# Kernel optimization log

Hardware: AMD Instinct MI355X
Metric: run time of the kernel (lower is better)

The kernel has to match this reference:

```python
import jax, jax.numpy as jnp
import numpy as np

K = 15  # window_size


def setup_inputs() -> dict:
    key = jax.random.key(0)
    k1, k2, k3, k4 = jax.random.split(key, 4)
    x = jax.random.normal(k1, (8, 256, 240, 240), dtype=jnp.float32)
    wq = jax.random.normal(k2, (144, 256), dtype=jnp.float32) * (1.0 / np.sqrt(256))
    wk = jax.random.normal(k3, (144, 256), dtype=jnp.float32) * (1.0 / np.sqrt(256))
    wproj = jax.random.normal(k4, (256, 256), dtype=jnp.float32) * (1.0 / np.sqrt(256))
    return {"x": x, "wq": wq, "wk": wk, "wproj": wproj}


def _pnlm(x, wq, wk, wproj):
    b, c, h, w = x.shape
    ph, pw = (-h) % K, (-w) % K
    if ph or pw:
        x_pad = jnp.pad(x, ((0, 0), (0, 0), (0, ph), (0, pw)), mode='reflect')
    else:
        x_pad = x
    H, W = x_pad.shape[2], x_pad.shape[3]
    nh, nw = H // K, W // K
    N = K * K  # tokens per window
    # blockify: (B,C,H,W) -> (B*nh*nw, C, N)
    blocks = (x_pad.reshape(b, c, nh, K, nw, K)
              .transpose(0, 2, 4, 1, 3, 5)
              .reshape(b * nh * nw, c, N))
    q = jnp.einsum('ec,bcn->bne', wq, blocks)   # (B', N, E)
    km = jnp.einsum('ec,bcm->bem', wk, blocks)  # (B', E, N)
    att = jnp.einsum('bne,bem->bnm', q, km)     # (B', N, N)
    scale = 1.0 / jnp.sqrt(jnp.asarray(q.shape[-1], dtype=att.dtype))
    att = jax.nn.softmax(att * scale, axis=-1)
    y = jnp.einsum('bnm,bcm->bcn', att, blocks)  # att @ V, V = blocks^T
    y = jnp.einsum('oc,bcn->bon', wproj, y)      # 1x1 proj_out
    # unblockify: (B', C, N) -> (B, C, H, W)
    y = (y.reshape(b, nh, nw, c, K, K)
         .transpose(0, 3, 1, 4, 2, 5)
         .reshape(b, c, H, W))
    y = y[:, :, :h, :w]
    return x + y


def reference(x, wq, wk, wproj):
    return _pnlm(x, wq, wk, wproj)
```

## Files before the change

### kernel.cpp

```cpp
#include <hip/hip_runtime.h>


typedef __bf16 bf16x8 __attribute__((ext_vector_type(8)));
typedef float  f32x4  __attribute__((ext_vector_type(4)));

#define MFMA(a,b,c) __builtin_amdgcn_mfma_f32_16x16x32_bf16((a),(b),(c),0,0,0)

#define QK_ROW 320
#define KL_STRIDE 168
#define XBB_ROW 240

__device__ __forceinline__ unsigned short f2bf(float f){
  union { float f; unsigned int u; } v; v.f = f;
  unsigned int r = v.u + 0x7FFFu + ((v.u >> 16) & 1u);
  return (unsigned short)(r >> 16);
}
__device__ __forceinline__ float bf2f(unsigned short u){
  union { unsigned int u; float f; } v; v.u = ((unsigned int)u) << 16;
  return v.f;
}
__device__ __forceinline__ int swz(int row, int col){
  return row*256 + ((((col >> 3) ^ (row & 7)) << 3) | (col & 7));
}
__device__ __forceinline__ int swzC(int row, int col){
  return row*256 + (col ^ ((((row >> 3) ^ row) & 7) << 3));
}
__device__ __forceinline__ bf16x8 ld_frag_lds(const unsigned short* p, int idx){
  uint4 v = *(const uint4*)(p + idx);
  return __builtin_bit_cast(bf16x8, v);
}
__device__ __forceinline__ bf16x8 ld_frag_b(const void* p){
  uint4 v = *(const uint4*)(p);
  return __builtin_bit_cast(bf16x8, v);
}

__device__ __forceinline__ void repack_frag(const unsigned int* plo, const unsigned int* phi,
                                            uint4* outf, int lane){
  const int nn = lane & 15, hh = lane >> 4;
  const int sla = nn + 32*(hh & 1);
  const int slb = sla + 16;
  const bool up = hh >= 2;
  #pragma unroll
  for (int k = 0; k < 8; ++k){
    unsigned int a0 = (unsigned int)__shfl((int)plo[2*k],   sla);
    unsigned int a1 = (unsigned int)__shfl((int)plo[2*k+1], sla);
    unsigned int b0 = (unsigned int)__shfl((int)phi[2*k],   sla);
    unsigned int b1 = (unsigned int)__shfl((int)phi[2*k+1], sla);
    unsigned int c0 = (unsigned int)__shfl((int)plo[2*k],   slb);
    unsigned int c1 = (unsigned int)__shfl((int)plo[2*k+1], slb);
    unsigned int d0 = (unsigned int)__shfl((int)phi[2*k],   slb);
    unsigned int d1 = (unsigned int)__shfl((int)phi[2*k+1], slb);
    outf[k] = make_uint4(up?a1:a0, up?b1:b0, up?c1:c0, up?d1:d0);
  }
}

__global__ __launch_bounds__(256) void k_w(
    const float* __restrict__ wq, const float* __restrict__ wk,
    const float* __restrict__ wproj,
    unsigned short* __restrict__ wqb, unsigned short* __restrict__ wkb,
    unsigned short* __restrict__ wpb)
{
  int i = blockIdx.x*256 + threadIdx.x;
  if (i < 20480){
    int e = i >> 7, c = (i & 127)*2;
    unsigned int v = 0;
    if (e < 144) v = (unsigned int)f2bf(wq[e*256+c]) | ((unsigned int)f2bf(wq[e*256+c+1]) << 16);
    *(unsigned int*)(wqb + (size_t)i*2) = v;
  } else if (i < 40960){
    int j = i - 20480;
    int e = j >> 7, c = (j & 127)*2;
    unsigned int v = 0;
    if (e < 144) v = (unsigned int)f2bf(wk[e*256+c]) | ((unsigned int)f2bf(wk[e*256+c+1]) << 16);
    *(unsigned int*)(wkb + (size_t)j*2) = v;
  } else if (i < 73728){
    int l = i - 40960;
    int o = l >> 7, c = (l & 127)*2;
    *(unsigned int*)(wpb + (size_t)l*2) =
        (unsigned int)f2bf(wproj[o*256+c]) | ((unsigned int)f2bf(wproj[o*256+c+1]) << 16);
  }
}

__global__ __launch_bounds__(256) void k_xb(
    const float* __restrict__ x, unsigned short* __restrict__ xbb)
{
  __shared__ unsigned short xs[8*15*240];
  const int wg = blockIdx.x;
  const int cg = wg & 31;
  const int th = (wg >> 5) & 15;
  const int b  = wg >> 9;
  const int tid = threadIdx.x;

  const float* xb = x + ((size_t)b*256 + cg*8)*57600 + th*15*240;
  for (int i = tid; i < 8*15*120; i += 256){
    int c = i / 1800;
    int rem = i - c*1800;
    int r = rem / 120, p2 = rem - r*120;
    float2 v = *(const float2*)(xb + (size_t)c*57600 + r*240 + p2*2);
    *(unsigned int*)(&xs[(c*15 + r)*240 + p2*2]) =
        (unsigned int)f2bf(v.x) | ((unsigned int)f2bf(v.y) << 16);
  }
  __syncthreads();

  for (int i = tid; i < 8*16*30; i += 256){
    int c = i / 480;
    int rem = i - c*480;
    int tw = rem / 30, ch = rem - tw*30;
    union { unsigned short u16[8]; uint4 u4; } pk;
    #pragma unroll
    for (int j = 0; j < 8; ++j){
      int m = ch*8 + j;
      int r = m / 15, s = m - r*15;
      pk.u16[j] = (m <= 224) ? xs[(c*15 + r)*240 + tw*15 + s] : (unsigned short)0;
    }
    *(uint4*)(xbb + ((size_t)(b*256 + th*16 + tw)*256 + cg*8 + c)*XBB_ROW + ch*8) = pk.u4;
  }
}

__global__ __launch_bounds__(512,4) void k_fused(
    const unsigned short* __restrict__ xbb,
    const unsigned short* __restrict__ wqb, const unsigned short* __restrict__ wkb,
    const unsigned short* __restrict__ wpb,
    unsigned short* __restrict__ qkws, float* __restrict__ out)
{
  __shared__ __align__(16) unsigned short S[40960];
  unsigned short* xt  = S;
  unsigned short* wqs = S;
  unsigned short* wks = S + 8192;
  unsigned short* kl  = S;
  unsigned short* xl  = S;
  unsigned short* wl  = S;
  unsigned int*  hwp  = (unsigned int*)(S + 40320);
  const int wg = blockIdx.x;
  const int b  = wg >> 8;
  const int th = (wg >> 4) & 15, tw = wg & 15;
  const int h0 = th*15, w0 = tw*15;
  const int tid = threadIdx.x;
  const int lane = tid & 63, wave = tid >> 6;
  const int col  = lane & 15, hi = lane >> 4;
  const size_t obase = (size_t)b * 256 * 57600;
  const unsigned short* qkb = qkws + (size_t)b * 57600 * QK_ROW;
  const unsigned short* xbw = xbb + (size_t)wg * (256*XBB_ROW);

  if (tid < 240){
    int ms = tid <= 224 ? tid : 224;
    hwp[tid] = (unsigned int)((h0 + ms/15)*240 + w0 + ms%15);
  }

  bf16x8 af[2][8];
  #pragma unroll 1
  for (int half = 0; half < 2; ++half){
    if (half) __syncthreads();
    for (int i = tid; i < 256*16; i += 512){
      int c = i >> 4, m8 = i & 15;
      int m = half*128 + m8*8;
      if (m + 8 <= 240){
        uint4 v = *(const uint4*)(xbw + (size_t)c*XBB_ROW + m);
        const unsigned short* pv = (const unsigned short*)&v;
        #pragma unroll
        for (int j = 0; j < 8; ++j)
          xt[swzC(m8*8 + j, c)] = pv[j];
      }
    }
    __syncthreads();
    const int rloc = wave*16 + col;
    if (half == 0){
      #pragma unroll
      for (int k = 0; k < 8; ++k)
        af[0][k] = ld_frag_lds(xt, swzC(rloc, k*32 + hi*8));
    } else {
      #pragma unroll
      for (int k = 0; k < 8; ++k)
        af[1][k] = ld_frag_lds(xt, swzC(rloc, k*32 + hi*8));
    }
  }
  __syncthreads();

  #pragma unroll 1
  for (int eg = 0; eg < 5; ++eg){
    if (eg) __syncthreads();
    for (int i = tid; i < 32*32; i += 512){
      int e_l = i >> 5, c8 = (i & 31)*8;
      size_t off = (size_t)(eg*32 + e_l)*256 + c8;
      *(uint4*)(&wqs[swz(e_l, c8)]) = *(const uint4*)(wqb + off);
      *(uint4*)(&wks[swz(e_l, c8)]) = *(const uint4*)(wkb + off);
    }
    __syncthreads();
    #pragma unroll
    for (int h2 = 0; h2 < 2; ++h2){
      const int t = h2*8 + wave;
      if (t < 15){
        #pragma unroll
        for (int et = 0; et < 2; ++et){
          f32x4 aq = {0.f,0.f,0.f,0.f}, ak = {0.f,0.f,0.f,0.f};
          const int el = et*16 + col;
          #pragma unroll
          for (int k = 0; k < 8; ++k){
            int idx = swz(el, k*32 + hi*8);
            bf16x8 bq = ld_frag_lds(wqs, idx);
            bf16x8 bk = ld_frag_lds(wks, idx);
            aq = MFMA(af[h2][k], bq, aq);
            ak = MFMA(af[h2][k], bk, ak);
          }
          const int e_out = eg*32 + et*16 + col;
          #pragma unroll
          for (int jj = 0; jj < 4; ++jj){
            int m_px = t*16 + hi*4 + jj;
            if (m_px <= 224){
              int hw = (h0 + m_px/15)*240 + w0 + m_px%15;
              size_t row = ((size_t)b*57600 + hw)*QK_ROW;
              qkws[row + e_out]       = f2bf(aq[jj]);
              qkws[row + 160 + e_out] = f2bf(ak[jj]);
            }
          }
        }
      }
    }
  }
  __syncthreads();

  for (int i = tid; i < 240*20; i += 512){
    int m = i / 20, eb = i - m*20;
    *(uint4*)(&kl[m*KL_STRIDE + eb*8]) =
        *(const uint4*)(qkb + (size_t)hwp[m]*QK_ROW + 160 + eb*8);
  }
  __syncthreads();

  uint4 attf[2][8];
  #pragma unroll
  for (int slot = 0; slot < 2; ++slot){
    const int nt = wave + slot*8;
    if (nt < 15){
      const int n  = nt*16 + col;
      const int na = n <= 224 ? n : 224;
      const unsigned short* qrow = qkb + (size_t)hwp[na]*QK_ROW;
      bf16x8 qf[5];
      #pragma unroll
      for (int c = 0; c < 5; ++c)
        qf[c] = ld_frag_b(qrow + c*32 + hi*8);
      f32x4 at[15];
      #pragma unroll
      for (int T = 0; T < 15; ++T){
        f32x4 acc = {0.f,0.f,0.f,0.f};
        #pragma unroll
        for (int c = 0; c < 5; ++c){
          bf16x8 kf = ld_frag_lds(kl, (T*16 + col)*KL_STRIDE + c*32 + hi*8);
          acc = MFMA(kf, qf[c], acc);
        }
        at[T] = acc;
      }
      const float sc = 0.12022458674074695f;
      float M = -3.0e38f;
      #pragma unroll
      for (int T = 0; T < 15; ++T){
        #pragma unroll
        for (int jj = 0; jj < 4; ++jj){
          int m = T*16 + hi*4 + jj;
          if (m <= 224) M = fmaxf(M, at[T][jj]*sc);
        }
      }
      M = fmaxf(M, __shfl_xor(M, 16));
      M = fmaxf(M, __shfl_xor(M, 32));
      float Ssum = 0.f;
      #pragma unroll
      for (int T = 0; T < 15; ++T){
        #pragma unroll
        for (int jj = 0; jj < 4; ++jj){
          int m = T*16 + hi*4 + jj;
          float v = (m <= 224) ? exp2f(at[T][jj]*sc - M) : 0.f;
          at[T][jj] = v; Ssum += v;
        }
      }
      Ssum += __shfl_xor(Ssum, 16);
      Ssum += __shfl_xor(Ssum, 32);
      const float inv = 1.0f / Ssum;
      unsigned int plo[16], phi[16];
      #pragma unroll
      for (int T = 0; T < 15; ++T){
        plo[T] = (unsigned int)f2bf(at[T][0]*inv) | ((unsigned int)f2bf(at[T][1]*inv) << 16);
        phi[T] = (unsigned int)f2bf(at[T][2]*inv) | ((unsigned int)f2bf(at[T][3]*inv) << 16);
      }
      plo[15] = 0u; phi[15] = 0u;
      repack_frag(plo, phi, attf[slot], lane);
    }
  }

  int pixs[2];
  #pragma unroll
  for (int slot = 0; slot < 2; ++slot){
    const int n = (wave + slot*8)*16 + col;
    pixs[slot] = (n <= 224) ? (int)hwp[n] : -1;
  }

  unsigned int ylo[2][16], yhi[2][16];
  #pragma unroll
  for (int half = 0; half < 2; ++half){
    __syncthreads();
    for (int i = tid; i < 128*32; i += 512){
      int c = i >> 5, m8 = i & 31;
      uint4 v = make_uint4(0u,0u,0u,0u);
      if (m8 < 30)
        v = *(const uint4*)(xbw + (size_t)(half*128 + c)*XBB_ROW + m8*8);
      *(uint4*)(&xl[swz(c, m8*8)]) = v;
    }
    __syncthreads();
    #pragma unroll
    for (int slot = 0; slot < 2; ++slot){
      const int nt = wave + slot*8;
      if (nt < 15){
        #pragma unroll
        for (int ct = 0; ct < 8; ++ct){
          f32x4 acc = {0.f,0.f,0.f,0.f};
          #pragma unroll
          for (int k = 0; k < 8; ++k){
            bf16x8 xf = ld_frag_lds(xl, swz(ct*16 + col, k*32 + hi*8));
            acc = MFMA(xf, __builtin_bit_cast(bf16x8, attf[slot][k]), acc);
          }
          ylo[slot][half*8 + ct] = (unsigned int)f2bf(acc[0]) | ((unsigned int)f2bf(acc[1]) << 16);
          yhi[slot][half*8 + ct] = (unsigned int)f2bf(acc[2]) | ((unsigned int)f2bf(acc[3]) << 16);
        }
      }
    }
  }

  uint4 y1f[2][8];
  #pragma unroll
  for (int slot = 0; slot < 2; ++slot){
    const int nt = wave + slot*8;
    if (nt < 15)
      repack_frag(ylo[slot], yhi[slot], y1f[slot], lane);
  }

  #pragma unroll 1
  for (int oe2 = 0; oe2 < 4; ++oe2){
    __syncthreads();
    for (int i = tid; i < 64*32; i += 512){
      int olr = i >> 5, c8 = (i & 31)*8;
      *(uint4*)(&wl[swz(olr, c8)]) =
          *(const uint4*)(wpb + (size_t)(oe2*64 + olr)*256 + c8);
    }
    __syncthreads();
    #pragma unroll
    for (int ot = 0; ot < 4; ++ot){
      bf16x8 awf[8];
      const int olr = ot*16 + col;
      #pragma unroll
      for (int k = 0; k < 8; ++k)
        awf[k] = ld_frag_lds(wl, swz(olr, k*32 + hi*8));
      #pragma unroll
      for (int slot = 0; slot < 2; ++slot){
        const int nt = wave + slot*8;
        if (nt < 15){
          f32x4 y2 = {0.f,0.f,0.f,0.f};
          #pragma unroll
          for (int k = 0; k < 8; ++k)
            y2 = MFMA(awf[k], __builtin_bit_cast(bf16x8, y1f[slot][k]), y2);
          const int n = nt*16 + col;
          if (n <= 224){
            const size_t pix = (size_t)pixs[slot];
            #pragma unroll
            for (int jj = 0; jj < 4; ++jj){
              int o = oe2*64 + ot*16 + hi*4 + jj;
              float xr = bf2f(xbw[(size_t)o*XBB_ROW + n]);
              out[obase + (size_t)o*57600 + pix] = y2[jj] + xr;
            }
          }
        }
      }
    }
  }
}

__global__ __launch_bounds__(512) void k_qk(
    const float* __restrict__ x, const float* __restrict__ wq,
    const float* __restrict__ wk,
    unsigned short* __restrict__ qkws)
{
  __shared__ __align__(16) unsigned short S[32768];
  unsigned short* xt  = S;
  unsigned short* wqs = S;
  unsigned short* wks = S + 8192;
  const int wg  = blockIdx.x;
  const int b   = wg / 450;
  const int hw0 = (wg % 450) * 128;
  const int tid = threadIdx.x;
  const int lane = tid & 63, wave = tid >> 6;
  const int col  = lane & 15, hi = lane >> 4;

  {
    const float* xb = x + (size_t)b * 256 * 57600 + hw0;
    const int hw_l = tid & 127;
    #pragma unroll 4
    for (int i = 0; i < 32; ++i){
      int c = ((tid >> 7) * 32 + i) * 2;
      float f0 = xb[(size_t)c     * 57600 + hw_l];
      float f1 = xb[(size_t)(c+1) * 57600 + hw_l];
      *(unsigned int*)(&xt[swz(hw_l, c)]) =
          (unsigned int)f2bf(f0) | ((unsigned int)f2bf(f1) << 16);
    }
  }
  __syncthreads();

  bf16x8 af[8];
  const int arow = wave*16 + col;
  #pragma unroll
  for (int k = 0; k < 8; ++k)
    af[k] = ld_frag_lds(xt, swz(arow, k*32 + hi*8));

  const size_t orow_base = (size_t)b*57600 + hw0 + wave*16;

  for (int eg = 0; eg < 5; ++eg){
    __syncthreads();
    for (int i = 0; i < 8; ++i){
      int idx = tid + i*512;
      int e_l = idx >> 7, c = (idx & 127) * 2;
      int e = eg*32 + e_l;
      float2 vq = make_float2(0.f,0.f), vk = make_float2(0.f,0.f);
      if (e < 144){
        vq = *(const float2*)(wq + (size_t)e*256 + c);
        vk = *(const float2*)(wk + (size_t)e*256 + c);
      }
      *(unsigned int*)(&wqs[swz(e_l, c)]) =
          (unsigned int)f2bf(vq.x) | ((unsigned int)f2bf(vq.y) << 16);
      *(unsigned int*)(&wks[swz(e_l, c)]) =
          (unsigned int)f2bf(vk.x) | ((unsigned int)f2bf(vk.y) << 16);
    }
    __syncthreads();
    #pragma unroll
    for (int etl = 0; etl < 2; ++etl){
      f32x4 aq = {0.f,0.f,0.f,0.f}, ak = {0.f,0.f,0.f,0.f};
      const int el = etl*16 + col;
      #pragma unroll
      for (int k = 0; k < 8; ++k){
        int idx = swz(el, k*32 + hi*8);
        bf16x8 bq = ld_frag_lds(wqs, idx);
        bf16x8 bk = ld_frag_lds(wks, idx);
        aq = MFMA(af[k], bq, aq);
        ak = MFMA(af[k], bk, ak);
      }
      const int e_out = eg*32 + etl*16 + col;
      #pragma unroll
      for (int jj = 0; jj < 4; ++jj){
        size_t row = orow_base + hi*4 + jj;
        qkws[row*QK_ROW + e_out]       = f2bf(aq[jj]);
        qkws[row*QK_ROW + 160 + e_out] = f2bf(ak[jj]);
      }
    }
  }
}

__global__ __launch_bounds__(512,4) void k_attn_s(
    const float* __restrict__ x, const float* __restrict__ wproj,
    const unsigned short* __restrict__ qkws, float* __restrict__ out)
{
  __shared__ __align__(16) unsigned short S[40320 + 480];
  unsigned short* kl = S;
  unsigned short* xl = S;
  unsigned short* wl = S + 32768;
  unsigned int*  hwp = (unsigned int*)(S + 40320);
  const int wg = blockIdx.x;
  const int b  = wg >> 8;
  const int th = (wg >> 4) & 15, tw = wg & 15;
  const int h0 = th*15, w0 = tw*15;
  const int tid = threadIdx.x;
  const int lane = tid & 63, wave = tid >> 6;
  const int col  = lane & 15, hi = lane >> 4;
  const size_t xbase = (size_t)b * 256 * 57600;
  const unsigned short* qkb = qkws + (size_t)b * 57600 * QK_ROW;

  if (tid < 240){
    int ms = tid <= 224 ? tid : 224;
    hwp[tid] = (unsigned int)((h0 + ms/15)*240 + w0 + ms%15);
  }
  __syncthreads();

  for (int i = tid; i < 240*20; i += 512){
    int m = i / 20, eb = i - m*20;
    *(uint4*)(&kl[m*KL_STRIDE + eb*8]) =
        *(const uint4*)(qkb + (size_t)hwp[m]*QK_ROW + 160 + eb*8);
  }
  __syncthreads();

  uint4 attf[2][8];
  #pragma unroll
  for (int slot = 0; slot < 2; ++slot){
    const int nt = wave + slot*8;
    if (nt < 15){
      const int n  = nt*16 + col;
      const int na = n <= 224 ? n : 224;
      const unsigned short* qrow = qkb + (size_t)hwp[na]*QK_ROW;
      bf16x8 qf[5];
      #pragma unroll
      for (int c = 0; c < 5; ++c)
        qf[c] = ld_frag_b(qrow + c*32 + hi*8);
      f32x4 at[15];
      #pragma unroll
      for (int T = 0; T < 15; ++T){
        f32x4 acc = {0.f,0.f,0.f,0.f};
        #pragma unroll
        for (int c = 0; c < 5; ++c){
          bf16x8 kf = ld_frag_lds(kl, (T*16 + col)*KL_STRIDE + c*32 + hi*8);
          acc = MFMA(kf, qf[c], acc);
        }
        at[T] = acc;
      }
      const float sc = 0.12022458674074695f;
      float M = -3.0e38f;
      #pragma unroll
      for (int T = 0; T < 15; ++T){
        #pragma unroll
        for (int jj = 0; jj < 4; ++jj){
          int m = T*16 + hi*4 + jj;
          if (m <= 224) M = fmaxf(M, at[T][jj]*sc);
        }
      }
      M = fmaxf(M, __shfl_xor(M, 16));
      M = fmaxf(M, __shfl_xor(M, 32));
      float Ssum = 0.f;
      #pragma unroll
      for (int T = 0; T < 15; ++T){
        #pragma unroll
        for (int jj = 0; jj < 4; ++jj){
          int m = T*16 + hi*4 + jj;
          float v = (m <= 224) ? exp2f(at[T][jj]*sc - M) : 0.f;
          at[T][jj] = v; Ssum += v;
        }
      }
      Ssum += __shfl_xor(Ssum, 16);
      Ssum += __shfl_xor(Ssum, 32);
      const float inv = 1.0f / Ssum;
      unsigned int plo[16], phi[16];
      #pragma unroll
      for (int T = 0; T < 15; ++T){
        plo[T] = (unsigned int)f2bf(at[T][0]*inv) | ((unsigned int)f2bf(at[T][1]*inv) << 16);
        phi[T] = (unsigned int)f2bf(at[T][2]*inv) | ((unsigned int)f2bf(at[T][3]*inv) << 16);
      }
      plo[15] = 0u; phi[15] = 0u;
      repack_frag(plo, phi, attf[slot], lane);
    }
  }

  unsigned int ylo[2][16], yhi[2][16];
  #pragma unroll
  for (int half = 0; half < 2; ++half){
    __syncthreads();
    for (int i = tid; i < 128*128; i += 512){
      int c = i >> 7, m = (i & 127)*2;
      int m0 = m <= 224 ? m : 224;
      float f0 = (m     <= 224) ? x[xbase + (size_t)(half*128 + c)*57600 + hwp[m0]]   : 0.f;
      float f1 = (m + 1 <= 224) ? x[xbase + (size_t)(half*128 + c)*57600 + hwp[m0+1]] : 0.f;
      *(unsigned int*)(&xl[swz(c, m)]) =
          (unsigned int)f2bf(f0) | ((unsigned int)f2bf(f1) << 16);
    }
    __syncthreads();
    #pragma unroll
    for (int slot = 0; slot < 2; ++slot){
      const int nt = wave + slot*8;
      if (nt < 15){
        #pragma unroll
        for (int ct = 0; ct < 8; ++ct){
          f32x4 acc = {0.f,0.f,0.f,0.f};
          #pragma unroll
          for (int k = 0; k < 8; ++k){
            bf16x8 xf = ld_frag_lds(xl, swz(ct*16 + col, k*32 + hi*8));
            acc = MFMA(xf, __builtin_bit_cast(bf16x8, attf[slot][k]), acc);
          }
          ylo[slot][half*8 + ct] = (unsigned int)f2bf(acc[0]) | ((unsigned int)f2bf(acc[1]) << 16);
          yhi[slot][half*8 + ct] = (unsigned int)f2bf(acc[2]) | ((unsigned int)f2bf(acc[3]) << 16);
        }
      }
    }
  }

  uint4 y1f[2][8];
  #pragma unroll
  for (int slot = 0; slot < 2; ++slot){
    const int nt = wave + slot*8;
    if (nt < 15)
      repack_frag(ylo[slot], yhi[slot], y1f[slot], lane);
  }

  #pragma unroll 1
  for (int oe = 0; oe < 16; ++oe){
    __syncthreads();
    for (int i = tid; i < 16*128; i += 512){
      int olr = i >> 7, c = (i & 127)*2;
      const float* wr = wproj + (size_t)(oe*16 + olr)*256 + c;
      *(unsigned int*)(&wl[swz(olr, c)]) =
          (unsigned int)f2bf(wr[0]) | ((unsigned int)f2bf(wr[1]) << 16);
    }
    __syncthreads();
    bf16x8 awf[8];
    #pragma unroll
    for (int k = 0; k < 8; ++k)
      awf[k] = ld_frag_lds(wl, swz(col, k*32 + hi*8));
    #pragma unroll
    for (int slot = 0; slot < 2; ++slot){
      const int nt = wave + slot*8;
      if (nt < 15){
        f32x4 y2 = {0.f,0.f,0.f,0.f};
        #pragma unroll
        for (int k = 0; k < 8; ++k)
          y2 = MFMA(awf[k], __builtin_bit_cast(bf16x8, y1f[slot][k]), y2);
        const int n = nt*16 + col;
        if (n <= 224){
          const size_t pix = hwp[n];
          #pragma unroll
          for (int jj = 0; jj < 4; ++jj){
            int o = oe*16 + hi*4 + jj;
            const size_t idx = xbase + (size_t)o*57600 + pix;
            out[idx] = y2[jj] + x[idx];
          }
        }
      }
    }
  }
}

extern "C" void kernel_launch(void* const* d_in, const int* in_sizes, int n_in,
                              void* d_out, int out_size, void* d_ws, size_t ws_size,
                              hipStream_t stream)
{
  const float* x     = (const float*)d_in[0];
  const float* wq    = (const float*)d_in[1];
  const float* wk    = (const float*)d_in[2];
  const float* wproj = (const float*)d_in[3];
  float* out = (float*)d_out;
  (void)in_sizes; (void)n_in; (void)out_size;

  const size_t QKWS_B = (size_t)8*57600*QK_ROW*2;
  const size_t XBB_B  = (size_t)8*256*256*XBB_ROW*2;
  const size_t WB_ALL = (size_t)(160*256 + 160*256 + 256*256)*2;
  unsigned short* qkws = (unsigned short*)d_ws;

  if (ws_size >= QKWS_B + XBB_B + WB_ALL){
    unsigned short* xbb = (unsigned short*)((char*)d_ws + QKWS_B);
    unsigned short* wqb = (unsigned short*)((char*)d_ws + QKWS_B + XBB_B);
    unsigned short* wkb = wqb + 160*256;
    unsigned short* wpb = wkb + 160*256;
    k_w    <<<dim3(288),  dim3(256), 0, stream>>>(wq, wk, wproj, wqb, wkb, wpb);
    k_xb   <<<dim3(4096), dim3(256), 0, stream>>>(x, xbb);
    k_fused<<<dim3(2048), dim3(512), 0, stream>>>(xbb, wqb, wkb, wpb, qkws, out);
  } else {
    k_qk    <<<dim3(3600), dim3(512), 0, stream>>>(x, wq, wk, qkws);
    k_attn_s<<<dim3(2048), dim3(512), 0, stream>>>(x, wproj, qkws, out);
  }
}
```

Measured before the change: 945.7 us.

## Keep Q/K projections on-chip instead of round-tripping through global workspace

The fused kernel no longer writes Q and K to a global workspace and reads them back. Q is staged in LDS and loaded into registers, and K is held in registers and then written to LDS for the attention MFMAs. Weight fragments now come straight from global/L2 rather than being staged through LDS in five synchronized chunks, so several barriers disappear. The cost is higher register pressure (the K fragments and Q fragments are kept live), which could lower occupancy under the 512x4 launch bound.

```diff
diff --git a/kernel.cpp b/kernel.cpp
--- a/kernel.cpp
+++ b/kernel.cpp
@@ -120,16 +120,15 @@
     const unsigned short* __restrict__ xbb,
     const unsigned short* __restrict__ wqb, const unsigned short* __restrict__ wkb,
     const unsigned short* __restrict__ wpb,
-    unsigned short* __restrict__ qkws, float* __restrict__ out)
+    float* __restrict__ out)
 {
-  __shared__ __align__(16) unsigned short S[40960];
-  unsigned short* xt  = S;
-  unsigned short* wqs = S;
-  unsigned short* wks = S + 8192;
-  unsigned short* kl  = S;
-  unsigned short* xl  = S;
-  unsigned short* wl  = S;
-  unsigned int*  hwp  = (unsigned int*)(S + 40320);
+  __shared__ __align__(16) unsigned short S[40800];
+  unsigned short* xt = S;
+  unsigned short* ql = S;
+  unsigned short* kl = S;
+  unsigned short* xl = S;
+  unsigned short* wl = S;
+  unsigned int*  hwp = (unsigned int*)(S + 40320);
   const int wg = blockIdx.x;
   const int b  = wg >> 8;
   const int th = (wg >> 4) & 15, tw = wg & 15;
@@ -138,7 +137,6 @@
   const int lane = tid & 63, wave = tid >> 6;
   const int col  = lane & 15, hi = lane >> 4;
   const size_t obase = (size_t)b * 256 * 57600;
-  const unsigned short* qkb = qkws + (size_t)b * 57600 * QK_ROW;
   const unsigned short* xbw = xbb + (size_t)wg * (256*XBB_ROW);
 
   if (tid < 240){
@@ -153,13 +151,13 @@
     for (int i = tid; i < 256*16; i += 512){
       int c = i >> 4, m8 = i & 15;
       int m = half*128 + m8*8;
-      if (m + 8 <= 240){
-        uint4 v = *(const uint4*)(xbw + (size_t)c*XBB_ROW + m);
-        const unsigned short* pv = (const unsigned short*)&v;
-        #pragma unroll
-        for (int j = 0; j < 8; ++j)
-          xt[swzC(m8*8 + j, c)] = pv[j];
-      }
+      uint4 v = make_uint4(0u,0u,0u,0u);
+      if (m + 8 <= 240)
+        v = *(const uint4*)(xbw + (size_t)c*XBB_ROW + m);
+      const unsigned short* pv = (const unsigned short*)&v;
+      #pragma unroll
+      for (int j = 0; j < 8; ++j)
+        xt[swzC(m8*8 + j, c)] = pv[j];
     }
     __syncthreads();
     const int rloc = wave*16 + col;
@@ -175,68 +173,87 @@
   }
   __syncthreads();
 
-  #pragma unroll 1
+  unsigned int Klo[2][5][2], Khi[2][5][2];
+  #pragma unroll
   for (int eg = 0; eg < 5; ++eg){
-    if (eg) __syncthreads();
-    for (int i = tid; i < 32*32; i += 512){
-      int e_l = i >> 5, c8 = (i & 31)*8;
-      size_t off = (size_t)(eg*32 + e_l)*256 + c8;
-      *(uint4*)(&wqs[swz(e_l, c8)]) = *(const uint4*)(wqb + off);
-      *(uint4*)(&wks[swz(e_l, c8)]) = *(const uint4*)(wkb + off);
-    }
-    __syncthreads();
-    #pragma unroll
-    for (int h2 = 0; h2 < 2; ++h2){
-      const int t = h2*8 + wave;
-      if (t < 15){
-        #pragma unroll
-        for (int et = 0; et < 2; ++et){
-          f32x4 aq = {0.f,0.f,0.f,0.f}, ak = {0.f,0.f,0.f,0.f};
-          const int el = et*16 + col;
-          #pragma unroll
-          for (int k = 0; k < 8; ++k){
-            int idx = swz(el, k*32 + hi*8);
-            bf16x8 bq = ld_frag_lds(wqs, idx);
-            bf16x8 bk = ld_frag_lds(wks, idx);
-            aq = MFMA(af[h2][k], bq, aq);
-            ak = MFMA(af[h2][k], bk, ak);
-          }
-          const int e_out = eg*32 + et*16 + col;
-          #pragma unroll
-          for (int jj = 0; jj < 4; ++jj){
-            int m_px = t*16 + hi*4 + jj;
-            if (m_px <= 224){
-              int hw = (h0 + m_px/15)*240 + w0 + m_px%15;
-              size_t row = ((size_t)b*57600 + hw)*QK_ROW;
-              qkws[row + e_out]       = f2bf(aq[jj]);
-              qkws[row + 160 + e_out] = f2bf(ak[jj]);
-            }
-          }
-        }
-      }
-    }
-  }
-  __syncthreads();
-
-  for (int i = tid; i < 240*20; i += 512){
-    int m = i / 20, eb = i - m*20;
-    *(uint4*)(&kl[m*KL_STRIDE + eb*8]) =
-        *(const uint4*)(qkb + (size_t)hwp[m]*QK_ROW + 160 + eb*8);
-  }
-  __syncthreads();
-
-  uint4 attf[2][8];
+    #pragma unroll
+    for (int et = 0; et < 2; ++et){
+      const int ebase = eg*32 + et*16 + col;
+      const unsigned short* wqr = wqb + (size_t)ebase*256 + hi*8;
+      const unsigned short* wkr = wkb + (size_t)ebase*256 + hi*8;
+      f32x4 aq0 = {0.f,0.f,0.f,0.f}, ak0 = {0.f,0.f,0.f,0.f};
+      f32x4 aq1 = {0.f,0.f,0.f,0.f}, ak1 = {0.f,0.f,0.f,0.f};
+      #pragma unroll
+      for (int k = 0; k < 8; ++k){
+        bf16x8 bq = ld_frag_b(wqr + k*32);
+        bf16x8 bk = ld_frag_b(wkr + k*32);
+        aq0 = MFMA(af[0][k], bq, aq0);
+        ak0 = MFMA(af[0][k], bk, ak0);
+        aq1 = MFMA(af[1][k], bq, aq1);
+        ak1 = MFMA(af[1][k], bk, ak1);
+      }
+      {
+        const int r0 = (wave*16 + hi*4)*KL_STRIDE + ebase;
+        ql[r0                ] = f2bf(aq0[0]);
+        ql[r0 +   KL_STRIDE  ] = f2bf(aq0[1]);
+        ql[r0 + 2*KL_STRIDE  ] = f2bf(aq0[2]);
+        ql[r0 + 3*KL_STRIDE  ] = f2bf(aq0[3]);
+        if (wave < 7){
+          const int r1 = ((8+wave)*16 + hi*4)*KL_STRIDE + ebase;
+          ql[r1               ] = f2bf(aq1[0]);
+          ql[r1 +   KL_STRIDE ] = f2bf(aq1[1]);
+          ql[r1 + 2*KL_STRIDE ] = f2bf(aq1[2]);
+          ql[r1 + 3*KL_STRIDE ] = f2bf(aq1[3]);
+        }
+      }
+      Klo[0][eg][et] = (unsigned int)f2bf(ak0[0]) | ((unsigned int)f2bf(ak0[1]) << 16);
+      Khi[0][eg][et] = (unsigned int)f2bf(ak0[2]) | ((unsigned int)f2bf(ak0[3]) << 16);
+      Klo[1][eg][et] = (unsigned int)f2bf(ak1[0]) | ((unsigned int)f2bf(ak1[1]) << 16);
+      Khi[1][eg][et] = (unsigned int)f2bf(ak1[2]) | ((unsigned int)f2bf(ak1[3]) << 16);
+    }
+  }
+  __syncthreads();
+
+  uint4 qf[2][5];
   #pragma unroll
   for (int slot = 0; slot < 2; ++slot){
     const int nt = wave + slot*8;
     if (nt < 15){
       const int n  = nt*16 + col;
       const int na = n <= 224 ? n : 224;
-      const unsigned short* qrow = qkb + (size_t)hwp[na]*QK_ROW;
-      bf16x8 qf[5];
       #pragma unroll
       for (int c = 0; c < 5; ++c)
-        qf[c] = ld_frag_b(qrow + c*32 + hi*8);
+        qf[slot][c] = *(const uint4*)(ql + na*KL_STRIDE + c*32 + hi*8);
+    }
+  }
+  __syncthreads();
+
+  #pragma unroll
+  for (int eg = 0; eg < 5; ++eg){
+    #pragma unroll
+    for (int et = 0; et < 2; ++et){
+      const int ebase = eg*32 + et*16 + col;
+      const int r0 = (wave*16 + hi*4)*KL_STRIDE + ebase;
+      kl[r0                ] = (unsigned short)(Klo[0][eg][et] & 0xFFFFu);
+      kl[r0 +   KL_STRIDE  ] = (unsigned short)(Klo[0][eg][et] >> 16);
+      kl[r0 + 2*KL_STRIDE  ] = (unsigned short)(Khi[0][eg][et] & 0xFFFFu);
+      kl[r0 + 3*KL_STRIDE  ] = (unsigned short)(Khi[0][eg][et] >> 16);
+      if (wave < 7){
+        const int r1 = ((8+wave)*16 + hi*4)*KL_STRIDE + ebase;
+        kl[r1               ] = (unsigned short)(Klo[1][eg][et] & 0xFFFFu);
+        kl[r1 +   KL_STRIDE ] = (unsigned short)(Klo[1][eg][et] >> 16);
+        kl[r1 + 2*KL_STRIDE ] = (unsigned short)(Khi[1][eg][et] & 0xFFFFu);
+        kl[r1 + 3*KL_STRIDE ] = (unsigned short)(Khi[1][eg][et] >> 16);
+      }
+    }
+  }
+  __syncthreads();
+
+  uint4 attf[2][8];
+  #pragma unroll
+  for (int slot = 0; slot < 2; ++slot){
+    const int nt = wave + slot*8;
+    if (nt < 15){
       f32x4 at[15];
       #pragma unroll
       for (int T = 0; T < 15; ++T){
@@ -244,7 +261,7 @@
         #pragma unroll
         for (int c = 0; c < 5; ++c){
           bf16x8 kf = ld_frag_lds(kl, (T*16 + col)*KL_STRIDE + c*32 + hi*8);
-          acc = MFMA(kf, qf[c], acc);
+          acc = MFMA(kf, __builtin_bit_cast(bf16x8, qf[slot][c]), acc);
         }
         at[T] = acc;
       }
@@ -282,13 +299,6 @@
       plo[15] = 0u; phi[15] = 0u;
       repack_frag(plo, phi, attf[slot], lane);
     }
-  }
-
-  int pixs[2];
-  #pragma unroll
-  for (int slot = 0; slot < 2; ++slot){
-    const int n = (wave + slot*8)*16 + col;
-    pixs[slot] = (n <= 224) ? (int)hwp[n] : -1;
   }
 
   unsigned int ylo[2][16], yhi[2][16];
@@ -356,7 +366,7 @@
             y2 = MFMA(awf[k], __builtin_bit_cast(bf16x8, y1f[slot][k]), y2);
           const int n = nt*16 + col;
           if (n <= 224){
-            const size_t pix = (size_t)pixs[slot];
+            const size_t pix = hwp[n];
             #pragma unroll
             for (int jj = 0; jj < 4; ++jj){
               int o = oe2*64 + ot*16 + hi*4 + jj;
@@ -632,14 +642,14 @@
   const size_t WB_ALL = (size_t)(160*256 + 160*256 + 256*256)*2;
   unsigned short* qkws = (unsigned short*)d_ws;
 
-  if (ws_size >= QKWS_B + XBB_B + WB_ALL){
-    unsigned short* xbb = (unsigned short*)((char*)d_ws + QKWS_B);
-    unsigned short* wqb = (unsigned short*)((char*)d_ws + QKWS_B + XBB_B);
+  if (ws_size >= XBB_B + WB_ALL){
+    unsigned short* xbb = (unsigned short*)d_ws;
+    unsigned short* wqb = (unsigned short*)((char*)d_ws + XBB_B);
     unsigned short* wkb = wqb + 160*256;
     unsigned short* wpb = wkb + 160*256;
     k_w    <<<dim3(288),  dim3(256), 0, stream>>>(wq, wk, wproj, wqb, wkb, wpb);
     k_xb   <<<dim3(4096), dim3(256), 0, stream>>>(x, xbb);
-    k_fused<<<dim3(2048), dim3(512), 0, stream>>>(xbb, wqb, wkb, wpb, qkws, out);
+    k_fused<<<dim3(2048), dim3(512), 0, stream>>>(xbb, wqb, wkb, wpb, out);
   } else {
     k_qk    <<<dim3(3600), dim3(512), 0, stream>>>(x, wq, wk, qkws);
     k_attn_s<<<dim3(2048), dim3(512), 0, stream>>>(x, wproj, qkws, out);
```

Measured after the change: 1.160 ms. 22.6% more time.
